# Kernel tuning notes

Hardware: AMD Instinct MI355X
Metric: run time of the kernel (lower is better)

Reference implementation:

```python
import jax, jax.numpy as jnp
import numpy as np

H, HK, D, WIN = 16, 4, 128, 1024  # n_head, n_kv_head, head_dim, left window


def rmsnorm(x):
    eps = jnp.asarray(jnp.finfo(x.dtype).eps, x.dtype)
    return x * jax.lax.rsqrt(jnp.mean(x * x, axis=-1, keepdims=True) + eps)


def rope(x, cos, sin):
    d = x.shape[-1] // 2
    x1, x2 = x[..., :d], x[..., d:]
    return jnp.concatenate([x1 * cos + x2 * sin, x1 * -sin + x2 * cos], axis=-1)


def setup_inputs() -> dict:
    key = jax.random.key(0)
    ks = jax.random.split(key, 12)
    B, T, C = 4, 2048, 2048
    t = jnp.arange(T, dtype=jnp.float32)[:, None]
    inv = 1.0 / (10000.0 ** (jnp.arange(D // 2, dtype=jnp.float32) / (D // 2)))
    ang = t * inv[None, :]  # [T, D/2]
    return {
        "x": jax.random.normal(ks[0], (B, T, C), jnp.float32),
        "x0": jax.random.normal(ks[1], (B, T, C), jnp.float32),
        "ve": jnp.zeros((B, T, C), jnp.float32),  # unused in add_init_qkv branch
        "cos": jnp.cos(ang)[None, :, None, :],  # [1,T,1,D/2]
        "sin": jnp.sin(ang)[None, :, None, :],
        "Wq": jax.random.normal(ks[2], (H * D, C), jnp.float32) * 0.02,
        "Wk": jax.random.normal(ks[3], (HK * D, C), jnp.float32) * 0.02,
        "Wv": jax.random.normal(ks[4], (HK * D, C), jnp.float32) * 0.02,
        "Wproj": jax.random.normal(ks[5], (C, H * D), jnp.float32) * 0.02,
        "alpha_q": jnp.ones((1,), jnp.float32),
        "beta_q": jax.random.uniform(ks[6], (1,), jnp.float32),
        "alpha_k": jnp.ones((1,), jnp.float32),
        "beta_k": jax.random.uniform(ks[7], (1,), jnp.float32),
        "alpha_v": jnp.ones((1,), jnp.float32),
        "beta_v": jax.random.uniform(ks[8], (1,), jnp.float32),
    }


def reference(x, x0, ve, cos, sin, Wq, Wk, Wv, Wproj,
              alpha_q, beta_q, alpha_k, beta_k, alpha_v, beta_v):
    B, T, C = x.shape
    g = H // HK  # GQA group size

    q = (x @ Wq.T).reshape(B, T, H, D)
    k = (x @ Wk.T).reshape(B, T, HK, D)
    v = (x @ Wv.T).reshape(B, T, HK, D)
    v_init = v

    # is_target + add_init_qkv + learn_init_coeffs: blend with projections of norm(x0)
    x0n = rmsnorm(x0)
    cqx = (x0n @ Wq.T).reshape(B, T, H, D)
    ckx = (x0n @ Wk.T).reshape(B, T, HK, D)
    cvx = (x0n @ Wv.T).reshape(B, T, HK, D)
    q = alpha_q * q + beta_q * cqx
    k = alpha_k * k + beta_k * ckx
    v = alpha_v * v + beta_v * cvx

    # rotary + qk-norm + 1.2 scale
    q = rmsnorm(rope(q, cos, sin)) * 1.2
    k = rmsnorm(rope(k, cos, sin)) * 1.2

    qg = q.reshape(B, T, HK, g, D)
    scale = 1.0 / np.sqrt(D)
    scores = jnp.einsum('bqhgd,bkhd->bhgqk', qg, k) * scale  # [B,HK,g,T,T]
    i = jnp.arange(T)[:, None]
    j = jnp.arange(T)[None, :]
    mask = (j <= i) & (i - j <= WIN)
    scores = jnp.where(mask, scores, -jnp.inf)
    p = jax.nn.softmax(scores, axis=-1)
    y = jnp.einsum('bhgqk,bkhd->bqhgd', p, v).reshape(B, T, H * D)

    y = y @ Wproj.T
    return (y, v_init)
```

## Files before the change

kernel.cpp:

```cpp
#include <hip/hip_runtime.h>
#include <hip/hip_bf16.h>
#include <math.h>


using bf16 = __hip_bfloat16;
typedef __attribute__((ext_vector_type(8))) short bf16x8;
typedef __attribute__((ext_vector_type(4))) short bf16x4;
typedef __attribute__((ext_vector_type(4))) float f32x4;

constexpr int Bb = 4, Ts = 2048, Cc = 2048, NH = 16, NKV = 4, Dh = 128, WIN = 1024;
constexpr float EPS = 1.1920929e-07f;

__device__ __forceinline__ void gld16(void* lds, const void* g) {
  __builtin_amdgcn_global_load_lds(
      (__attribute__((address_space(1))) unsigned int*)((void*)g),
      (__attribute__((address_space(3))) unsigned int*)lds, 16, 0, 0);
}

__device__ __forceinline__ unsigned short bfbits(float f) {
  bf16 h = __float2bfloat16(f);
  return __builtin_bit_cast(unsigned short, h);
}

__device__ __forceinline__ void store_out(float* p, float v) { *p = v; }
__device__ __forceinline__ void store_out(bf16* p, float v) { *p = __float2bfloat16(v); }

__device__ __forceinline__ f32x4 mfma16(bf16x4 a, bf16x4 b, f32x4 c) {
#if __has_builtin(__builtin_amdgcn_mfma_f32_16x16x16bf16_1k)
  return __builtin_amdgcn_mfma_f32_16x16x16bf16_1k(a, b, c, 0, 0, 0);
#else
  bf16x8 a8 = {a[0], a[1], a[2], a[3], 0, 0, 0, 0};
  bf16x8 b8 = {b[0], b[1], b[2], b[3], 0, 0, 0, 0};
  return __builtin_amdgcn_mfma_f32_16x16x32_bf16(a8, b8, c, 0, 0, 0);
#endif
}

__global__ __launch_bounds__(256) void convert_w(const float* __restrict__ src,
                                                 bf16* __restrict__ dst, int n4) {
  int i = blockIdx.x * 256 + threadIdx.x;
  if (i < n4) {
    float4 v = ((const float4*)src)[i];
    ushort4 u;
    u.x = bfbits(v.x); u.y = bfbits(v.y); u.z = bfbits(v.z); u.w = bfbits(v.w);
    ((ushort4*)dst)[i] = u;
  }
}

__global__ __launch_bounds__(256) void prep(
    const float* __restrict__ x, const float* __restrict__ x0,
    const float* aq_p, const float* bq_p, const float* ak_p, const float* bk_p,
    bf16* __restrict__ xq, bf16* __restrict__ xk,
    bf16* __restrict__ xb, bf16* __restrict__ x0n) {
  const int row = blockIdx.x, tid = threadIdx.x;
  const float4* xr = (const float4*)(x + (size_t)row * Cc);
  const float4* nr = (const float4*)(x0 + (size_t)row * Cc);
  float4 xa[2], na[2];
  float ss = 0.f;
#pragma unroll
  for (int j = 0; j < 2; ++j) {
    xa[j] = xr[tid + j * 256];
    na[j] = nr[tid + j * 256];
    ss += na[j].x * na[j].x + na[j].y * na[j].y + na[j].z * na[j].z + na[j].w * na[j].w;
  }
#pragma unroll
  for (int o = 32; o; o >>= 1) ss += __shfl_xor(ss, o);
  __shared__ float red[4];
  if ((tid & 63) == 0) red[tid >> 6] = ss;
  __syncthreads();
  const float rms = rsqrtf((red[0] + red[1] + red[2] + red[3]) * (1.f / Cc) + EPS);
  const float aq = *aq_p, bq = *bq_p, ak = *ak_p, bk = *bk_p;
#pragma unroll
  for (int j = 0; j < 2; ++j) {
    const size_t base = (size_t)row * Cc + (size_t)(tid + j * 256) * 4;
    float nx[4] = {na[j].x * rms, na[j].y * rms, na[j].z * rms, na[j].w * rms};
    float xv[4] = {xa[j].x, xa[j].y, xa[j].z, xa[j].w};
    ushort4 uq, uk, ub, un;
    uq.x = bfbits(aq * xv[0] + bq * nx[0]); uq.y = bfbits(aq * xv[1] + bq * nx[1]);
    uq.z = bfbits(aq * xv[2] + bq * nx[2]); uq.w = bfbits(aq * xv[3] + bq * nx[3]);
    uk.x = bfbits(ak * xv[0] + bk * nx[0]); uk.y = bfbits(ak * xv[1] + bk * nx[1]);
    uk.z = bfbits(ak * xv[2] + bk * nx[2]); uk.w = bfbits(ak * xv[3] + bk * nx[3]);
    ub.x = bfbits(xv[0]); ub.y = bfbits(xv[1]); ub.z = bfbits(xv[2]); ub.w = bfbits(xv[3]);
    un.x = bfbits(nx[0]); un.y = bfbits(nx[1]); un.z = bfbits(nx[2]); un.w = bfbits(nx[3]);
    *(ushort4*)(xq + base) = uq;
    *(ushort4*)(xk + base) = uk;
    *(ushort4*)(xb + base) = ub;
    *(ushort4*)(x0n + base) = un;
  }
}

template <typename OutT>
__device__ __forceinline__ void gemm_body(
    const bf16* __restrict__ A, const bf16* __restrict__ W,
    OutT* __restrict__ C, int N, int K) {
  __shared__ unsigned short sA[128 * 64];
  __shared__ unsigned short sB[128 * 64];
  const int tid = threadIdx.x, wave = tid >> 6, lane = tid & 63;
  const int quad = lane >> 4, l15 = lane & 15;
  const int bm = blockIdx.x * 128, bn = blockIdx.y * 128;
  const int wm = (wave >> 1) * 64, wn = (wave & 1) * 64;
  const int srow = wave * 32 + (lane >> 3);
  const int scol = (lane & 7) * 8;

  f32x4 acc[4][4] = {};

  for (int k0 = 0; k0 < K; k0 += 64) {
#pragma unroll
    for (int i = 0; i < 4; ++i) {
      gld16(&sA[(wave * 32 + i * 8) * 64], &A[(size_t)(bm + srow + i * 8) * K + k0 + scol]);
      gld16(&sB[(wave * 32 + i * 8) * 64], &W[(size_t)(bn + srow + i * 8) * K + k0 + scol]);
    }
    __syncthreads();
#pragma unroll
    for (int kk = 0; kk < 2; ++kk) {
      bf16x8 af[4], bfr[4];
#pragma unroll
      for (int t = 0; t < 4; ++t)
        af[t] = *(const bf16x8*)&sA[(wm + t * 16 + l15) * 64 + kk * 32 + quad * 8];
#pragma unroll
      for (int t = 0; t < 4; ++t)
        bfr[t] = *(const bf16x8*)&sB[(wn + t * 16 + l15) * 64 + kk * 32 + quad * 8];
#pragma unroll
      for (int tm = 0; tm < 4; ++tm)
#pragma unroll
        for (int tn = 0; tn < 4; ++tn)
          acc[tm][tn] = __builtin_amdgcn_mfma_f32_16x16x32_bf16(af[tm], bfr[tn], acc[tm][tn], 0, 0, 0);
    }
    __syncthreads();
  }
#pragma unroll
  for (int tm = 0; tm < 4; ++tm)
#pragma unroll
    for (int tn = 0; tn < 4; ++tn)
#pragma unroll
      for (int r = 0; r < 4; ++r) {
        const int row = bm + wm + tm * 16 + quad * 4 + r;
        const int col = bn + wn + tn * 16 + l15;
        store_out(&C[(size_t)row * N + col], acc[tm][tn][r]);
      }
}

template <typename OutT>
__global__ __launch_bounds__(256) void gemm_bt(
    const bf16* __restrict__ A, const bf16* __restrict__ W,
    OutT* __restrict__ C, int N, int K) {
  gemm_body<OutT>(A, W, C, N, K);
}

struct GemmTriple { const bf16* A; const bf16* W; bf16* C; };
struct GemmTriple3 { GemmTriple t[3]; };

__global__ __launch_bounds__(256) void gemm_bt3(GemmTriple3 g, int N, int K) {
  const GemmTriple tr = g.t[blockIdx.z];
  gemm_body<bf16>(tr.A, tr.W, tr.C, N, K);
}

__global__ __launch_bounds__(256) void post_qk(
    const bf16* __restrict__ pre, const float* __restrict__ cosp,
    const float* __restrict__ sinp, bf16* __restrict__ outh, int nh, float mult) {
  const int wid = blockIdx.x * 4 + (threadIdx.x >> 6);
  const int lane = threadIdx.x & 63;
  const int h = wid % nh;
  const int bt = wid / nh;
  const int t = bt & (Ts - 1);
  const int b = bt >> 11;
  const size_t src = (size_t)bt * (size_t)(nh * Dh) + (size_t)h * Dh;
  float x1 = __bfloat162float(pre[src + lane]);
  float x2 = __bfloat162float(pre[src + 64 + lane]);
  float c = cosp[t * 64 + lane], s = sinp[t * 64 + lane];
  float o1 = x1 * c + x2 * s;
  float o2 = x2 * c - x1 * s;
  float ss = o1 * o1 + o2 * o2;
#pragma unroll
  for (int o = 32; o; o >>= 1) ss += __shfl_xor(ss, o);
  const float r = rsqrtf(ss * (1.f / Dh) + EPS) * mult;
  const size_t dst = ((size_t)(b * nh + h) * Ts + t) * Dh;
  outh[dst + lane] = __float2bfloat16(o1 * r);
  outh[dst + 64 + lane] = __float2bfloat16(o2 * r);
}

__global__ __launch_bounds__(256) void post_v(
    const bf16* __restrict__ vinit, const bf16* __restrict__ cvx,
    const float* av_p, const float* bv_p,
    bf16* __restrict__ vth, float* __restrict__ vout) {
  __shared__ unsigned short vt[128 * 65];
  const int t0 = blockIdx.x * 64;
  const int b = blockIdx.y >> 2, hk = blockIdx.y & 3;
  const float av = *av_p, bv = *bv_p;
  const int tid = threadIdx.x;
  for (int j = 0; j < 32; ++j) {
    const int e = j * 256 + tid;
    const int tl = e >> 7, d = e & 127;
    const size_t src = (size_t)(b * Ts + t0 + tl) * (NKV * Dh) + hk * Dh + d;
    const float vi = __bfloat162float(vinit[src]);
    const float cv = __bfloat162float(cvx[src]);
    vout[src] = vi;
    vt[d * 65 + tl] = bfbits(av * vi + bv * cv);
  }
  __syncthreads();
#pragma unroll
  for (int j = 0; j < 4; ++j) {
    const int g = j * 256 + tid;
    const int d = g >> 3, t8 = (g & 7) * 8;
    const unsigned short* p = &vt[d * 65 + t8];
    uint4 u;
    u.x = p[0] | ((unsigned int)p[1] << 16);
    u.y = p[2] | ((unsigned int)p[3] << 16);
    u.z = p[4] | ((unsigned int)p[5] << 16);
    u.w = p[6] | ((unsigned int)p[7] << 16);
    *(uint4*)&vth[((size_t)(b * NKV + hk) * Dh + d) * Ts + t0 + t8] = u;
  }
}

__global__ __launch_bounds__(256) void attn(
    const bf16* __restrict__ qh, const bf16* __restrict__ kh,
    const bf16* __restrict__ vth, bf16* __restrict__ att) {
  __shared__ unsigned short sK[64 * 128];
  __shared__ unsigned short sV[128 * 64];

  const int tid = threadIdx.x, wave = tid >> 6, lane = tid & 63;
  const int quad = lane >> 4, l15 = lane & 15;
  const int q0 = blockIdx.x * 128;
  const int b = blockIdx.y >> 4, h = blockIdx.y & 15, hk = h >> 2;

  const bf16* Qp = qh + (size_t)(b * NH + h) * Ts * Dh;
  const bf16* Kp = kh + (size_t)(b * NKV + hk) * Ts * Dh;
  const bf16* Vp = vth + (size_t)(b * NKV + hk) * Dh * Ts;

  const int qw = q0 + wave * 32;

  bf16x8 qf[2][4];
#pragma unroll
  for (int tm = 0; tm < 2; ++tm)
#pragma unroll
    for (int kk = 0; kk < 4; ++kk)
      qf[tm][kk] = *(const bf16x8*)&Qp[(size_t)(qw + tm * 16 + l15) * Dh + kk * 32 + quad * 8];

  f32x4 of[2][8] = {};
  float m_i[2] = {-__builtin_inff(), -__builtin_inff()};
  float l_i[2] = {0.f, 0.f};

  const int krow = lane >> 4, kgp = lane & 15;
  const int vrow = lane >> 3, vgp = lane & 7;

  const int jt_lo = q0 >= WIN ? (q0 - WIN) >> 6 : 0;
  const int jt_hi = (q0 + 127) >> 6;

  for (int jt = jt_lo; jt <= jt_hi; ++jt) {
    const int j0 = jt << 6;
    __syncthreads();
#pragma unroll
    for (int i = 0; i < 4; ++i) {
      const int row = wave * 16 + i * 4 + krow;
      gld16(&sK[(wave * 16 + i * 4) * 128],
            &Kp[(size_t)(j0 + row) * Dh + (kgp ^ (row & 15)) * 8]);
      const int d = wave * 32 + i * 8 + vrow;
      gld16(&sV[(wave * 32 + i * 8) * 64],
            &Vp[(size_t)d * Ts + j0 + (vgp ^ (d & 7)) * 8]);
    }
    __syncthreads();

    if (j0 > qw + 31 || qw > j0 + 63 + WIN) continue;

    f32x4 sfT[4][2];
#pragma unroll
    for (int tn = 0; tn < 4; ++tn) {
      bf16x8 kf[4];
#pragma unroll
      for (int kk = 0; kk < 4; ++kk)
        kf[kk] = *(const bf16x8*)&sK[(tn * 16 + l15) * 128 + (((kk * 4 + quad) ^ l15) * 8)];
#pragma unroll
      for (int tm = 0; tm < 2; ++tm) {
        f32x4 a = {};
#pragma unroll
        for (int kk = 0; kk < 4; ++kk)
          a = __builtin_amdgcn_mfma_f32_16x16x32_bf16(kf[kk], qf[tm][kk], a, 0, 0, 0);
        sfT[tn][tm] = a;
      }
    }

    float alpha[2];
    bf16x4 pf[2][4];
#pragma unroll
    for (int tm = 0; tm < 2; ++tm) {
      const int dq = (qw + tm * 16 + l15) - (j0 + quad * 4);
      float mloc = -__builtin_inff();
#pragma unroll
      for (int tn = 0; tn < 4; ++tn)
#pragma unroll
        for (int r = 0; r < 4; ++r) {
          const unsigned diff = (unsigned)(dq - tn * 16 - r);
          float s = (diff <= (unsigned)WIN) ? sfT[tn][tm][r] : -__builtin_inff();
          sfT[tn][tm][r] = s;
          mloc = fmaxf(mloc, s);
        }
      mloc = fmaxf(mloc, __shfl_xor(mloc, 16));
      mloc = fmaxf(mloc, __shfl_xor(mloc, 32));
      const float mnew = fmaxf(m_i[tm], mloc);
      alpha[tm] = __builtin_amdgcn_exp2f(m_i[tm] - mnew);
      m_i[tm] = mnew;
      float rs = 0.f;
#pragma unroll
      for (int tn = 0; tn < 4; ++tn) {
        bf16x4 p4;
#pragma unroll
        for (int r = 0; r < 4; ++r) {
          const float p = __builtin_amdgcn_exp2f(sfT[tn][tm][r] - mnew);
          rs += p;
          p4[r] = (short)bfbits(p);
        }
        pf[tm][tn] = p4;
      }
      rs += __shfl_xor(rs, 16);
      rs += __shfl_xor(rs, 32);
      l_i[tm] = l_i[tm] * alpha[tm] + rs;
    }

#pragma unroll
    for (int tm = 0; tm < 2; ++tm) {
      float ar[4];
#pragma unroll
      for (int r = 0; r < 4; ++r) ar[r] = __shfl(alpha[tm], quad * 4 + r);
#pragma unroll
      for (int dn = 0; dn < 8; ++dn)
#pragma unroll
        for (int r = 0; r < 4; ++r) of[tm][dn][r] *= ar[r];
    }

#pragma unroll
    for (int tn = 0; tn < 4; ++tn) {
      const int gsw = (tn * 2) ^ (l15 & 7);
#pragma unroll
      for (int dn = 0; dn < 8; ++dn) {
        const int d = dn * 16 + l15;
        const bf16x4 vf = *(const bf16x4*)&sV[d * 64 + ((gsw ^ (quad >> 1)) * 8) + (quad & 1) * 4];
        of[0][dn] = mfma16(pf[0][tn], vf, of[0][dn]);
        of[1][dn] = mfma16(pf[1][tn], vf, of[1][dn]);
      }
    }
  }

#pragma unroll
  for (int tm = 0; tm < 2; ++tm) {
#pragma unroll
    for (int r = 0; r < 4; ++r) {
      const float lr = __shfl(l_i[tm], quad * 4 + r);
      const float inv = 1.f / lr;
      const int qr = qw + tm * 16 + quad * 4 + r;
      bf16* dst = att + (size_t)(b * Ts + qr) * (NH * Dh) + h * Dh;
#pragma unroll
      for (int dn = 0; dn < 8; ++dn)
        dst[dn * 16 + l15] = __float2bfloat16(of[tm][dn][r] * inv);
    }
  }
}

extern "C" void kernel_launch(void* const* d_in, const int* in_sizes, int n_in,
                              void* d_out, int out_size, void* d_ws, size_t ws_size,
                              hipStream_t stream) {
  const float* x = (const float*)d_in[0];
  const float* x0 = (const float*)d_in[1];
  const float* cosp = (const float*)d_in[3];
  const float* sinp = (const float*)d_in[4];
  const float* Wq = (const float*)d_in[5];
  const float* Wk = (const float*)d_in[6];
  const float* Wv = (const float*)d_in[7];
  const float* Wp = (const float*)d_in[8];
  const float* aq = (const float*)d_in[9];
  const float* bq = (const float*)d_in[10];
  const float* ak = (const float*)d_in[11];
  const float* bk = (const float*)d_in[12];
  const float* av = (const float*)d_in[13];
  const float* bv = (const float*)d_in[14];

  char* ws = (char*)d_ws;
  const size_t MB = 1024ull * 1024;
  bf16* xq = (bf16*)(ws + 0 * MB);
  bf16* xk = (bf16*)(ws + 32 * MB);
  bf16* xb = (bf16*)(ws + 64 * MB);
  bf16* x0n = (bf16*)(ws + 96 * MB);
  bf16* vinit = (bf16*)(ws + 128 * MB);
  bf16* cvx = (bf16*)(ws + 136 * MB);
  bf16* Wqb = (bf16*)(ws + 144 * MB);
  bf16* Wkb = (bf16*)(ws + 152 * MB);
  bf16* Wvb = (bf16*)(ws + 154 * MB);
  bf16* Wpb = (bf16*)(ws + 156 * MB);
  bf16* att = xq;
  bf16* qh = xk;
  bf16* kh = xb;
  bf16* vth = (bf16*)(ws + 72 * MB);

  float* y = (float*)d_out;
  float* vout = (float*)d_out + (size_t)Bb * Ts * Cc;
  bf16* q_pre = (bf16*)d_out;
  bf16* k_pre = (bf16*)vout;

  convert_w<<<4096, 256, 0, stream>>>(Wq, Wqb, 1048576);
  convert_w<<<1024, 256, 0, stream>>>(Wk, Wkb, 262144);
  convert_w<<<1024, 256, 0, stream>>>(Wv, Wvb, 262144);
  convert_w<<<4096, 256, 0, stream>>>(Wp, Wpb, 1048576);

  prep<<<8192, 256, 0, stream>>>(x, x0, aq, bq, ak, bk, xq, xk, xb, x0n);

  gemm_bt<bf16><<<dim3(64, 16), 256, 0, stream>>>(xq, Wqb, q_pre, 2048, 2048);

  GemmTriple3 g3;
  g3.t[0] = {xk, Wkb, k_pre};
  g3.t[1] = {xb, Wvb, vinit};
  g3.t[2] = {x0n, Wvb, cvx};
  gemm_bt3<<<dim3(64, 4, 3), 256, 0, stream>>>(g3, 512, 2048);

  const float qmult = 1.2f * 0.08838834764831845f * 1.4426950408889634f;
  post_qk<<<32768, 256, 0, stream>>>(q_pre, cosp, sinp, qh, NH, qmult);
  post_qk<<<8192, 256, 0, stream>>>(k_pre, cosp, sinp, kh, NKV, 1.2f);
  post_v<<<dim3(32, 16), 256, 0, stream>>>(vinit, cvx, av, bv, vth, vout);

  attn<<<dim3(16, 64), 256, 0, stream>>>(qh, kh, vth, att);

  gemm_bt<float><<<dim3(64, 16), 256, 0, stream>>>(att, Wpb, y, 2048, 2048);
}
```

Measured before the change: 793.9 us.

## Merge small launches, swizzle attention blocks, skip masking and lazy rescale

Four weight-conversion launches become one, and the two q/k post-processing launches become one, which cuts launch overhead. The attention grid is remapped with a block swizzle to change the order blocks are scheduled and improve cache locality across heads. Inside attention, tiles lying fully inside the causal window skip the mask arithmetic. The online-softmax rescale is deferred when the new max exceeds the running max by no more than 8 in log2 units, skipping the multiply of the output accumulator. The deferred rescale lets probabilities grow up to 2^8 before normalization, which adds a small numerical risk with bf16 probabilities.

Result: no change. 787.0 us (-0.9%).

```diff
diff --git a/kernel.cpp b/kernel.cpp
--- a/kernel.cpp
+++ b/kernel.cpp
@@ -35,15 +35,24 @@
 #endif
 }
 
-__global__ __launch_bounds__(256) void convert_w(const float* __restrict__ src,
-                                                 bf16* __restrict__ dst, int n4) {
-  int i = blockIdx.x * 256 + threadIdx.x;
-  if (i < n4) {
-    float4 v = ((const float4*)src)[i];
-    ushort4 u;
-    u.x = bfbits(v.x); u.y = bfbits(v.y); u.z = bfbits(v.z); u.w = bfbits(v.w);
-    ((ushort4*)dst)[i] = u;
-  }
+__global__ __launch_bounds__(256) void convert_w4(
+    const float* __restrict__ s0, bf16* __restrict__ d0,
+    const float* __restrict__ s1, bf16* __restrict__ d1,
+    const float* __restrict__ s2, bf16* __restrict__ d2,
+    const float* __restrict__ s3, bf16* __restrict__ d3) {
+  const int bid = blockIdx.x;
+  const float* src;
+  bf16* dst;
+  int base;
+  if (bid < 4096)      { src = s0; dst = d0; base = 0; }
+  else if (bid < 5120) { src = s1; dst = d1; base = 4096; }
+  else if (bid < 6144) { src = s2; dst = d2; base = 5120; }
+  else                 { src = s3; dst = d3; base = 6144; }
+  const int i = (bid - base) * 256 + threadIdx.x;
+  float4 v = ((const float4*)src)[i];
+  ushort4 u;
+  u.x = bfbits(v.x); u.y = bfbits(v.y); u.z = bfbits(v.z); u.w = bfbits(v.w);
+  ((ushort4*)dst)[i] = u;
 }
 
 __global__ __launch_bounds__(256) void prep(
@@ -154,10 +163,18 @@
   gemm_body<bf16>(tr.A, tr.W, tr.C, N, K);
 }
 
-__global__ __launch_bounds__(256) void post_qk(
-    const bf16* __restrict__ pre, const float* __restrict__ cosp,
-    const float* __restrict__ sinp, bf16* __restrict__ outh, int nh, float mult) {
-  const int wid = blockIdx.x * 4 + (threadIdx.x >> 6);
+__global__ __launch_bounds__(256) void post_qk2(
+    const bf16* __restrict__ qpre, const bf16* __restrict__ kpre,
+    const float* __restrict__ cosp, const float* __restrict__ sinp,
+    bf16* __restrict__ qh, bf16* __restrict__ kh, float qmult) {
+  int bid = blockIdx.x;
+  const bf16* pre;
+  bf16* outh;
+  int nh;
+  float mult;
+  if (bid < 32768) { pre = qpre; outh = qh; nh = NH; mult = qmult; }
+  else { bid -= 32768; pre = kpre; outh = kh; nh = NKV; mult = 1.2f; }
+  const int wid = bid * 4 + (threadIdx.x >> 6);
   const int lane = threadIdx.x & 63;
   const int h = wid % nh;
   const int bt = wid / nh;
@@ -219,8 +236,11 @@
 
   const int tid = threadIdx.x, wave = tid >> 6, lane = tid & 63;
   const int quad = lane >> 4, l15 = lane & 15;
-  const int q0 = blockIdx.x * 128;
-  const int b = blockIdx.y >> 4, h = blockIdx.y & 15, hk = h >> 2;
+  const int lin = blockIdx.y * 16 + blockIdx.x;
+  const int swz = (lin & 7) * 128 + (lin >> 3);
+  const int q0 = (swz & 15) * 128;
+  const int by = swz >> 4;
+  const int b = by >> 4, h = by & 15, hk = h >> 2;
 
   const bf16* Qp = qh + (size_t)(b * NH + h) * Ts * Dh;
   const bf16* Kp = kh + (size_t)(b * NKV + hk) * Ts * Dh;
@@ -278,26 +298,43 @@
       }
     }
 
+    const bool full = (j0 + 63 <= qw) && (qw + 31 - j0 <= WIN);
+
     float alpha[2];
+    bool defer[2];
     bf16x4 pf[2][4];
 #pragma unroll
     for (int tm = 0; tm < 2; ++tm) {
-      const int dq = (qw + tm * 16 + l15) - (j0 + quad * 4);
       float mloc = -__builtin_inff();
-#pragma unroll
-      for (int tn = 0; tn < 4; ++tn)
-#pragma unroll
-        for (int r = 0; r < 4; ++r) {
-          const unsigned diff = (unsigned)(dq - tn * 16 - r);
-          float s = (diff <= (unsigned)WIN) ? sfT[tn][tm][r] : -__builtin_inff();
-          sfT[tn][tm][r] = s;
-          mloc = fmaxf(mloc, s);
-        }
+      if (full) {
+#pragma unroll
+        for (int tn = 0; tn < 4; ++tn)
+#pragma unroll
+          for (int r = 0; r < 4; ++r) mloc = fmaxf(mloc, sfT[tn][tm][r]);
+      } else {
+        const int dq = (qw + tm * 16 + l15) - (j0 + quad * 4);
+#pragma unroll
+        for (int tn = 0; tn < 4; ++tn)
+#pragma unroll
+          for (int r = 0; r < 4; ++r) {
+            const unsigned diff = (unsigned)(dq - tn * 16 - r);
+            float s = (diff <= (unsigned)WIN) ? sfT[tn][tm][r] : -__builtin_inff();
+            sfT[tn][tm][r] = s;
+            mloc = fmaxf(mloc, s);
+          }
+      }
       mloc = fmaxf(mloc, __shfl_xor(mloc, 16));
       mloc = fmaxf(mloc, __shfl_xor(mloc, 32));
-      const float mnew = fmaxf(m_i[tm], mloc);
-      alpha[tm] = __builtin_amdgcn_exp2f(m_i[tm] - mnew);
-      m_i[tm] = mnew;
+      defer[tm] = __all(mloc - m_i[tm] <= 8.f);
+      float mnew;
+      if (defer[tm]) {
+        mnew = m_i[tm];
+        alpha[tm] = 1.f;
+      } else {
+        mnew = fmaxf(m_i[tm], mloc);
+        alpha[tm] = __builtin_amdgcn_exp2f(m_i[tm] - mnew);
+        m_i[tm] = mnew;
+      }
       float rs = 0.f;
 #pragma unroll
       for (int tn = 0; tn < 4; ++tn) {
@@ -317,13 +354,15 @@
 
 #pragma unroll
     for (int tm = 0; tm < 2; ++tm) {
-      float ar[4];
-#pragma unroll
-      for (int r = 0; r < 4; ++r) ar[r] = __shfl(alpha[tm], quad * 4 + r);
-#pragma unroll
-      for (int dn = 0; dn < 8; ++dn)
-#pragma unroll
-        for (int r = 0; r < 4; ++r) of[tm][dn][r] *= ar[r];
+      if (!defer[tm]) {
+        float ar[4];
+#pragma unroll
+        for (int r = 0; r < 4; ++r) ar[r] = __shfl(alpha[tm], quad * 4 + r);
+#pragma unroll
+        for (int dn = 0; dn < 8; ++dn)
+#pragma unroll
+          for (int r = 0; r < 4; ++r) of[tm][dn][r] *= ar[r];
+      }
     }
 
 #pragma unroll
@@ -394,10 +433,7 @@
   bf16* q_pre = (bf16*)d_out;
   bf16* k_pre = (bf16*)vout;
 
-  convert_w<<<4096, 256, 0, stream>>>(Wq, Wqb, 1048576);
-  convert_w<<<1024, 256, 0, stream>>>(Wk, Wkb, 262144);
-  convert_w<<<1024, 256, 0, stream>>>(Wv, Wvb, 262144);
-  convert_w<<<4096, 256, 0, stream>>>(Wp, Wpb, 1048576);
+  convert_w4<<<10240, 256, 0, stream>>>(Wq, Wqb, Wk, Wkb, Wv, Wvb, Wp, Wpb);
 
   prep<<<8192, 256, 0, stream>>>(x, x0, aq, bq, ak, bk, xq, xk, xb, x0n);
 
@@ -410,8 +446,7 @@
   gemm_bt3<<<dim3(64, 4, 3), 256, 0, stream>>>(g3, 512, 2048);
 
   const float qmult = 1.2f * 0.08838834764831845f * 1.4426950408889634f;
-  post_qk<<<32768, 256, 0, stream>>>(q_pre, cosp, sinp, qh, NH, qmult);
-  post_qk<<<8192, 256, 0, stream>>>(k_pre, cosp, sinp, kh, NKV, 1.2f);
+  post_qk2<<<40960, 256, 0, stream>>>(q_pre, k_pre, cosp, sinp, qh, kh, qmult);
   post_v<<<dim3(32, 16), 256, 0, stream>>>(vinit, cvx, av, bv, vth, vout);
 
   attn<<<dim3(16, 64), 256, 0, stream>>>(qh, kh, vth, att);
```
